# Optimization experiments

Measured on AMD Instinct MI355X. Metric: run time of the kernel, lower is better.

## Reference

```python
import jax, jax.numpy as jnp
import numpy as np

NUM_SLOTS = 3
NUM_ORIENTS = 8
PATCH_SIZE = 81  # 9x9 board
BUY_SIZE = NUM_SLOTS * NUM_ORIENTS * PATCH_SIZE  # 1944
ACTIONS = 1 + PATCH_SIZE + BUY_SIZE  # 2026
NEG = -1.0e9
EPS = 1e-5

B = 4096
C_IN = 256
HID = 256


def setup_inputs() -> dict:
    key = jax.random.key(0)
    ks = jax.random.split(key, 12)
    s = 0.05
    return {
        "x": jax.random.normal(ks[0], (B, C_IN, 9, 9), jnp.float32),
        "action_mask": jax.random.randint(ks[1], (B, ACTIONS), 0, 2, dtype=jnp.int32),
        # p_conv: 1x1 conv, no bias (use_batch_norm=True) -> weight (HID, C_IN)
        "conv_w": jax.random.normal(ks[2], (HID, C_IN), jnp.float32) * s,
        # BatchNorm2d (inference form with running stats)
        "bn_gamma": jnp.ones((HID,), jnp.float32),
        "bn_beta": jnp.zeros((HID,), jnp.float32),
        "bn_mean": jax.random.normal(ks[3], (HID,), jnp.float32) * 0.1,
        "bn_var": jax.random.uniform(ks[4], (HID,), jnp.float32, 0.5, 1.5),
        "type_w": jax.random.normal(ks[5], (3, HID), jnp.float32) * s,
        "type_b": jnp.zeros((3,), jnp.float32),
        "patch_w": jax.random.normal(ks[6], (1, HID), jnp.float32) * s,
        "patch_b": jnp.zeros((1,), jnp.float32),
        "slot_w": jax.random.normal(ks[7], (NUM_SLOTS, HID), jnp.float32) * s,
        "slot_b": jnp.zeros((NUM_SLOTS,), jnp.float32),
        "orient_w": jax.random.normal(ks[8], (NUM_SLOTS * NUM_ORIENTS, HID), jnp.float32) * s,
        "orient_b": jnp.zeros((NUM_SLOTS * NUM_ORIENTS,), jnp.float32),
        "pos_w": jax.random.normal(ks[9], (NUM_SLOTS * NUM_ORIENTS, HID), jnp.float32) * s,
        "pos_b": jnp.zeros((NUM_SLOTS * NUM_ORIENTS,), jnp.float32),
    }


def _masked_logsoftmax(logits, mask_bool):
    lg = jnp.where(mask_bool, logits, NEG)
    return jnp.maximum(jax.nn.log_softmax(lg, axis=-1), -100.0)


def reference(x, action_mask, conv_w, bn_gamma, bn_beta, bn_mean, bn_var,
              type_w, type_b, patch_w, patch_b, slot_w, slot_b,
              orient_w, orient_b, pos_w, pos_b):
    b = x.shape[0]
    # 1x1 conv + BN (eval) + ReLU
    p = jnp.einsum('bchw,oc->bohw', x, conv_w)
    scale = bn_gamma * jax.lax.rsqrt(bn_var + EPS)
    p = jax.nn.relu(p * scale[None, :, None, None] + (bn_beta - bn_mean * scale)[None, :, None, None])
    p_mean = p.mean(axis=(2, 3))  # (B, HID)

    # masks from action_mask layout [pass | 81 patch | 1944 buy]
    am = action_mask > 0
    patch_mask = am[:, 1:1 + PATCH_SIZE]
    buy4d = am[:, 82:82 + BUY_SIZE].reshape(b, NUM_SLOTS, NUM_ORIENTS, PATCH_SIZE)
    type_mask = jnp.stack([am[:, 0], patch_mask.any(-1), buy4d.reshape(b, -1).any(-1)], axis=-1)
    orient_mask = buy4d.any(-1)
    slot_mask = orient_mask.any(-1)

    type_lp = _masked_logsoftmax(p_mean @ type_w.T + type_b, type_mask)          # (B,3)
    patch_logits = jnp.einsum('bchw,oc->bohw', p, patch_w).reshape(b, PATCH_SIZE) \
        + patch_b[0]
    patch_lp = _masked_logsoftmax(patch_logits, patch_mask)                       # (B,81)
    slot_lp = _masked_logsoftmax(p_mean @ slot_w.T + slot_b, slot_mask)           # (B,3)
    orient_lp = _masked_logsoftmax(
        (p_mean @ orient_w.T + orient_b).reshape(b, NUM_SLOTS, NUM_ORIENTS), orient_mask)
    pos_logits = (jnp.einsum('bchw,oc->bohw', p, pos_w) + pos_b[None, :, None, None]) \
        .reshape(b, NUM_SLOTS, NUM_ORIENTS, PATCH_SIZE)
    pos_lp = _masked_logsoftmax(pos_logits, buy4d)                                # (B,3,8,81)

    pass_lp = type_lp[:, 0:1]
    patch_joint = type_lp[:, 1:2] + patch_lp
    buy_joint = (type_lp[:, 2:3, None, None] + slot_lp[:, :, None, None]
                 + orient_lp[:, :, :, None] + pos_lp).reshape(b, BUY_SIZE)
    return jnp.concatenate([pass_lp, patch_joint, buy_joint], axis=1)  # (B, 2026)
```

## Files before the change

### kernel.cpp

```cpp
#include <hip/hip_runtime.h>

#define ACT 2026
#define NEGV -1.0e9f

typedef short short8 __attribute__((ext_vector_type(8)));
typedef float f32x4 __attribute__((ext_vector_type(4)));

__device__ __forceinline__ unsigned f2bf(float f) {
  unsigned u = __float_as_uint(f);
  return (u + 0x7FFFu + ((u >> 16) & 1u)) >> 16;
}

__device__ __forceinline__ unsigned cvtpk(float lo, float hi) {
  unsigned r;
  asm("v_cvt_pk_bf16_f32 %0, %1, %2" : "=v"(r) : "v"(lo), "v"(hi));
  return r;
}

#define GL16(gp, lp) __builtin_amdgcn_global_load_lds(                         \
    (const __attribute__((address_space(1))) void*)(gp),                       \
    (__attribute__((address_space(3))) void*)(lp), 16, 0, 0)

__global__ void prep_w_kernel(const float* __restrict__ conv_w,
                              const float* __restrict__ pos_w,
                              const float* __restrict__ patch_w,
                              unsigned short* __restrict__ wimg,
                              unsigned short* __restrict__ w2img) {
  int g = blockIdx.x * 256 + threadIdx.x;
  if (g < 8192) {
    int r = g & 15, gq = (g >> 4) & 3, mtg = (g >> 6) & 15, ks = g >> 10;
    const float* src = conv_w + (mtg * 16 + r) * 256 + ks * 32 + gq * 8;
    unsigned v0 = f2bf(src[0]) | (f2bf(src[1]) << 16);
    unsigned v1 = f2bf(src[2]) | (f2bf(src[3]) << 16);
    unsigned v2 = f2bf(src[4]) | (f2bf(src[5]) << 16);
    unsigned v3 = f2bf(src[6]) | (f2bf(src[7]) << 16);
    uint4 q; q.x = v0; q.y = v1; q.z = v2; q.w = v3;
    *(uint4*)(wimg + g * 8) = q;
  } else if (g < 9216) {
    int g2 = g - 8192;
    int r = g2 & 15, gq = (g2 >> 4) & 3, mt = (g2 >> 6) & 1, ks2 = g2 >> 7;
    int m2 = mt * 16 + r;
    int o0 = ks2 * 32 + gq * 8;
    unsigned short v[8];
#pragma unroll
    for (int e = 0; e < 8; ++e) {
      float f = 0.f;
      if (m2 < 24) f = pos_w[m2 * 256 + o0 + e];
      else if (m2 == 24) f = patch_w[o0 + e];
      v[e] = (unsigned short)f2bf(f);
    }
    uint4 q;
    q.x = (unsigned)v[0] | ((unsigned)v[1] << 16);
    q.y = (unsigned)v[2] | ((unsigned)v[3] << 16);
    q.z = (unsigned)v[4] | ((unsigned)v[5] << 16);
    q.w = (unsigned)v[6] | ((unsigned)v[7] << 16);
    *(uint4*)(w2img + g2 * 8) = q;
  }
}

__global__ __launch_bounds__(512, 4)
void policy_main(const float* __restrict__ x,
                 const int* __restrict__ am,
                 const unsigned short* __restrict__ wimg,
                 const unsigned short* __restrict__ w2img,
                 const float* __restrict__ bn_gamma, const float* __restrict__ bn_beta,
                 const float* __restrict__ bn_mean, const float* __restrict__ bn_var,
                 const float* __restrict__ type_w, const float* __restrict__ type_b,
                 const float* __restrict__ patch_b,
                 const float* __restrict__ slot_w, const float* __restrict__ slot_b,
                 const float* __restrict__ orient_w, const float* __restrict__ orient_b,
                 const float* __restrict__ pos_b,
                 float* __restrict__ out)
{
  __shared__ __align__(16) char s_big[66048];
  __shared__ __align__(16) float s_scale[256];
  __shared__ __align__(16) float s_bias[256];
  __shared__ __align__(16) float s_pmean[256];
  __shared__ float s_part[240];
  __shared__ float s_hl[30];
  __shared__ int s_omask[24];
  __shared__ int s_misc[6];

  char* f32buf = s_big;
  char* bfimg  = s_big + 41472;
  unsigned short* pT = (unsigned short*)s_big;
  float* s_out2 = (float*)s_big;

  const int tid = threadIdx.x;
  const int w  = tid >> 6;
  const int l  = tid & 63;
  const int b  = blockIdx.x;
  const float* xb = x + (size_t)b * (256 * 81);

  if (tid < 256) {
    float sc = bn_gamma[tid] * rsqrtf(bn_var[tid] + 1e-5f);
    s_scale[tid] = sc;
    s_bias[tid]  = bn_beta[tid] - bn_mean[tid] * sc;
  }

  const int kg = l >> 4;
  const int kr = l & 15;
  const int g4 = kg * 4;
  const int fragoff = (kr * 4 + kg) * 16;

  f32x4 acc[2][6];
#pragma unroll
  for (int i = 0; i < 2; ++i)
#pragma unroll
    for (int j = 0; j < 6; ++j) {
      f32x4 z = {0.f, 0.f, 0.f, 0.f};
      acc[i][j] = z;
    }

  auto STAGE = [&](int ks) {
    const char* g = (const char*)xb + ks * 10368;
    char* lb = f32buf + (ks & 3) * 10368;
    int o1 = w * 81;
    int o2 = o1 + 17;
    GL16(g + (o1 + l) * 16, lb + o1 * 16);
    GL16(g + (o2 + l) * 16, lb + o2 * 16);
  };

  auto TRX = [&](int t, int q) {
    const float* src = (const float*)(f32buf + (t & 3) * 10368);
    char* dst = bfimg + (t & 3) * 6144;
    int nt_ = q >> 6, kr_ = (q >> 2) & 15, kg_ = q & 3;
    const float* s = src + kg_ * 648 + nt_ * 16 + kr_;
    uint4 v;
    v.x = cvtpk(s[0],   s[81]);
    v.y = cvtpk(s[162], s[243]);
    v.z = cvtpk(s[324], s[405]);
    v.w = cvtpk(s[486], s[567]);
    *(uint4*)(dst + q * 16) = v;
  };
  auto TRANSPOSE2 = [&](int tA, int tB) {
    if (tid < 384) TRX(tA, tid);
    else           TRX(tB, tid - 384);
    if (tid < 256) TRX(tB, 128 + tid);
  };

  STAGE(0); STAGE(1); STAGE(2); STAGE(3);
  asm volatile("s_waitcnt vmcnt(4)" ::: "memory");
  __builtin_amdgcn_s_barrier();
  __builtin_amdgcn_sched_barrier(0);
  TRANSPOSE2(0, 1);
  asm volatile("s_waitcnt vmcnt(0)" ::: "memory");
  asm volatile("s_waitcnt lgkmcnt(0)" ::: "memory");
  __builtin_amdgcn_s_barrier();
  __builtin_amdgcn_sched_barrier(0);

  auto SUPER = [&](int s) {
    const int t0 = 2 * s, t1 = t0 + 1;
    short8 af[4];
    {
      const unsigned short* ab0 = wimg + t0 * 8192 + w * 1024 + kg * 128 + kr * 8;
      const unsigned short* ab1 = wimg + t1 * 8192 + w * 1024 + kg * 128 + kr * 8;
      af[0] = *(const short8*)(ab0);
      af[1] = *(const short8*)(ab0 + 512);
      af[2] = *(const short8*)(ab1);
      af[3] = *(const short8*)(ab1 + 512);
    }
    __builtin_amdgcn_sched_barrier(0);
    if (s < 2) {
      STAGE(t0 + 4);
      STAGE(t1 + 4);
    }
    if (s < 3) TRANSPOSE2(t0 + 2, t1 + 2);
    const char* bi0 = bfimg + (t0 & 3) * 6144;
    const char* bi1 = bfimg + (t1 & 3) * 6144;
    __builtin_amdgcn_s_setprio(1);
#pragma unroll
    for (int nt = 0; nt < 6; ++nt) {
      short8 bf = *(const short8*)(bi0 + nt * 1024 + fragoff);
      acc[0][nt] = __builtin_amdgcn_mfma_f32_16x16x32_bf16(af[0], bf, acc[0][nt], 0, 0, 0);
      acc[1][nt] = __builtin_amdgcn_mfma_f32_16x16x32_bf16(af[1], bf, acc[1][nt], 0, 0, 0);
    }
#pragma unroll
    for (int nt = 0; nt < 6; ++nt) {
      short8 bf = *(const short8*)(bi1 + nt * 1024 + fragoff);
      acc[0][nt] = __builtin_amdgcn_mfma_f32_16x16x32_bf16(af[2], bf, acc[0][nt], 0, 0, 0);
      acc[1][nt] = __builtin_amdgcn_mfma_f32_16x16x32_bf16(af[3], bf, acc[1][nt], 0, 0, 0);
    }
    __builtin_amdgcn_s_setprio(0);
    if (s < 3) {
      asm volatile("s_waitcnt vmcnt(0)" ::: "memory");
      asm volatile("s_waitcnt lgkmcnt(0)" ::: "memory");
      __builtin_amdgcn_s_barrier();
      __builtin_amdgcn_sched_barrier(0);
    } else {
      __syncthreads();
    }
  };

  SUPER(0); SUPER(1); SUPER(2); SUPER(3);

#pragma unroll
  for (int mi = 0; mi < 2; ++mi) {
    int ob = w * 32 + mi * 16 + g4;
    float sc0 = s_scale[ob], sc1 = s_scale[ob + 1], sc2 = s_scale[ob + 2], sc3 = s_scale[ob + 3];
    float bi0 = s_bias[ob],  bi1 = s_bias[ob + 1],  bi2 = s_bias[ob + 2],  bi3 = s_bias[ob + 3];
    float vs0 = 0.f, vs1 = 0.f, vs2 = 0.f, vs3 = 0.f;
    int ks2 = ob >> 5;
    int j2  = (ob >> 3) & 3;
    int e0  = ob & 7;
    char* pbase = (char*)pT + ks2 * 6144 + j2 * 256 + kr * 16 + e0 * 2;
#pragma unroll
    for (int nt = 0; nt < 6; ++nt) {
      float v0 = fmaxf(acc[mi][nt][0] * sc0 + bi0, 0.f);
      float v1 = fmaxf(acc[mi][nt][1] * sc1 + bi1, 0.f);
      float v2 = fmaxf(acc[mi][nt][2] * sc2 + bi2, 0.f);
      float v3 = fmaxf(acc[mi][nt][3] * sc3 + bi3, 0.f);
      if (nt < 5 || kr == 0) { vs0 += v0; vs1 += v1; vs2 += v2; vs3 += v3; }
      uint2 pvv;
      pvv.x = cvtpk(v0, v1);
      pvv.y = cvtpk(v2, v3);
      *(uint2*)(pbase + nt * 1024) = pvv;
    }
    float vv[4] = {vs0, vs1, vs2, vs3};
#pragma unroll
    for (int i = 0; i < 4; ++i) {
      float s = vv[i];
      s += __shfl_xor(s, 1);
      s += __shfl_xor(s, 2);
      s += __shfl_xor(s, 4);
      s += __shfl_xor(s, 8);
      vv[i] = s;
    }
    if (kr == 0) {
      s_pmean[ob]     = vv[0] * (1.f / 81.f);
      s_pmean[ob + 1] = vv[1] * (1.f / 81.f);
      s_pmean[ob + 2] = vv[2] * (1.f / 81.f);
      s_pmean[ob + 3] = vv[3] * (1.f / 81.f);
    }
  }
  __syncthreads();

  const int* amr = am + (size_t)b * ACT;
  const int mt  = w & 1;
  const int ntb = (w >> 1) * 3;
  f32x4 acc2[3];
#pragma unroll
  for (int t = 0; t < 3; ++t) { f32x4 z = {0.f, 0.f, 0.f, 0.f}; acc2[t] = z; }

  if (w < 4) {
#pragma unroll
    for (int ks2 = 0; ks2 < 8; ++ks2) {
      const unsigned short* ap = w2img + ((ks2 * 2 + mt) * 4 + kg) * 128 + kr * 8;
      short8 a2 = *(const short8*)ap;
#pragma unroll
      for (int t = 0; t < 3; ++t) {
        const short8* bp = (const short8*)((const char*)pT + ks2 * 6144 + (ntb + t) * 1024 + kg * 256 + kr * 16);
        acc2[t] = __builtin_amdgcn_mfma_f32_16x16x32_bf16(a2, *bp, acc2[t], 0, 0, 0);
      }
    }
  } else {
    for (int t = w - 4; t < 25; t += 4) {
      int off = (t < 24) ? (82 + t * 81) : 1;
      int v1 = amr[off + l];
      int v2 = (l < 17) ? amr[off + 64 + l] : 0;
      unsigned long long bal = __ballot((v1 | v2) != 0);
      if (l == 0) {
        int any = (bal != 0ULL) ? 1 : 0;
        if (t < 24) s_omask[t] = any; else s_misc[0] = any;
      }
    }
    int hh = tid - 256;
    if (hh < 240) {
      int h = hh >> 3, seg = hh & 7;
      const float* wp = (h < 3) ? (type_w + h * 256)
                      : (h < 6) ? (slot_w + (h - 3) * 256)
                                : (orient_w + (h - 6) * 256);
      float p = 0.f;
      int base = seg * 32;
#pragma unroll 8
      for (int e = 0; e < 32; ++e) p += s_pmean[base + e] * wp[base + e];
      s_part[hh] = p;
    }
  }
  __syncthreads();

  if (w < 4) {
#pragma unroll
    for (int t = 0; t < 3; ++t) {
      int hw = (ntb + t) * 16 + kr;
      int m2 = mt * 16 + g4;
#pragma unroll
      for (int i = 0; i < 4; ++i)
        s_out2[(m2 + i) * 104 + hw] = acc2[t][i];
    }
  }
  if (tid < 30) {
    float a = 0.f;
#pragma unroll
    for (int e = 0; e < 8; ++e) a += s_part[tid * 8 + e];
    a += (tid < 3) ? type_b[tid] : (tid < 6) ? slot_b[tid - 3] : orient_b[tid - 6];
    s_hl[tid] = a;
  }
  if (tid == 32) {
    int sa0 = 0, sa1 = 0, sa2 = 0;
#pragma unroll
    for (int rr = 0; rr < 8; ++rr) { sa0 |= s_omask[rr]; sa1 |= s_omask[8 + rr]; sa2 |= s_omask[16 + rr]; }
    s_misc[1] = sa0; s_misc[2] = sa1; s_misc[3] = sa2;
    s_misc[4] = sa0 | sa1 | sa2;
  }
  __syncthreads();

  float tlp0, tlp1, tlp2;
  {
    int mk0 = amr[0] > 0, mk1 = s_misc[0], mk2 = s_misc[4];
    float g0 = mk0 ? s_hl[0] : NEGV;
    float g1 = mk1 ? s_hl[1] : NEGV;
    float g2 = mk2 ? s_hl[2] : NEGV;
    float m = fmaxf(fmaxf(g0, g1), g2);
    float ls = m + __logf(__expf(g0 - m) + __expf(g1 - m) + __expf(g2 - m));
    tlp0 = fmaxf(g0 - ls, -100.f);
    tlp1 = fmaxf(g1 - ls, -100.f);
    tlp2 = fmaxf(g2 - ls, -100.f);
  }
  float slp[3];
  {
    float g[3]; float m = -3.0e38f;
#pragma unroll
    for (int s = 0; s < 3; ++s) { g[s] = s_misc[1 + s] ? s_hl[3 + s] : NEGV; m = fmaxf(m, g[s]); }
    float sum = 0.f;
#pragma unroll
    for (int s = 0; s < 3; ++s) sum += __expf(g[s] - m);
    float ls = m + __logf(sum);
#pragma unroll
    for (int s = 0; s < 3; ++s) slp[s] = fmaxf(g[s] - ls, -100.f);
  }

  float* ob_out = out + (size_t)b * ACT;
  for (int t = w; t < 25; t += 8) {
    int off = (t < 24) ? (82 + t * 81) : 1;
    float badd = (t < 24) ? pos_b[t] : patch_b[0];
    int a1 = amr[off + l];
    int a2v = (l < 17) ? amr[off + 64 + l] : 0;
    float lg1 = (a1 > 0) ? (s_out2[t * 104 + l] + badd) : NEGV;
    float lg2 = (l < 17 && a2v > 0) ? (s_out2[t * 104 + 64 + l] + badd) : NEGV;
    float mx = fmaxf(lg1, (l < 17) ? lg2 : -3.0e38f);
#pragma unroll
    for (int mm = 1; mm < 64; mm <<= 1) mx = fmaxf(mx, __shfl_xor(mx, mm));
    float sm = __expf(lg1 - mx) + ((l < 17) ? __expf(lg2 - mx) : 0.f);
#pragma unroll
    for (int mm = 1; mm < 64; mm <<= 1) sm += __shfl_xor(sm, mm);
    float lse = mx + __logf(sm);
    float lp1 = fmaxf(lg1 - lse, -100.f);
    float lp2 = fmaxf(lg2 - lse, -100.f);
    float addj; int obase;
    if (t < 24) {
      int sl = t >> 3;
      float g[8]; float m = -3.0e38f;
#pragma unroll
      for (int rr = 0; rr < 8; ++rr) {
        g[rr] = s_omask[sl * 8 + rr] ? s_hl[6 + sl * 8 + rr] : NEGV;
        m = fmaxf(m, g[rr]);
      }
      float sum = 0.f;
#pragma unroll
      for (int rr = 0; rr < 8; ++rr) sum += __expf(g[rr] - m);
      float ls = m + __logf(sum);
      float olp_t = fmaxf(g[t & 7] - ls, -100.f);
      addj = tlp2 + slp[sl] + olp_t;
      obase = 82 + t * 81;
    } else {
      addj = tlp1;
      obase = 1;
    }
    ob_out[obase + l] = addj + lp1;
    if (l < 17) ob_out[obase + 64 + l] = addj + lp2;
    if (t == 24 && l == 0) ob_out[0] = tlp0;
  }
}

extern "C" void kernel_launch(void* const* d_in, const int* in_sizes, int n_in,
                              void* d_out, int out_size, void* d_ws, size_t ws_size,
                              hipStream_t stream) {
  (void)in_sizes; (void)n_in; (void)out_size; (void)ws_size;
  const float* x        = (const float*)d_in[0];
  const int*   amask    = (const int*)d_in[1];
  const float* conv_w   = (const float*)d_in[2];
  const float* bn_gamma = (const float*)d_in[3];
  const float* bn_beta  = (const float*)d_in[4];
  const float* bn_mean  = (const float*)d_in[5];
  const float* bn_var   = (const float*)d_in[6];
  const float* type_w   = (const float*)d_in[7];
  const float* type_b   = (const float*)d_in[8];
  const float* patch_w  = (const float*)d_in[9];
  const float* patch_b  = (const float*)d_in[10];
  const float* slot_w   = (const float*)d_in[11];
  const float* slot_b   = (const float*)d_in[12];
  const float* orient_w = (const float*)d_in[13];
  const float* orient_b = (const float*)d_in[14];
  const float* pos_w    = (const float*)d_in[15];
  const float* pos_b    = (const float*)d_in[16];
  float* outp = (float*)d_out;

  unsigned short* wimg  = (unsigned short*)d_ws;
  unsigned short* w2img = wimg + 65536;

  prep_w_kernel<<<36, 256, 0, stream>>>(conv_w, pos_w, patch_w, wimg, w2img);
  policy_main<<<4096, 512, 0, stream>>>(x, amask, wimg, w2img,
                                        bn_gamma, bn_beta, bn_mean, bn_var,
                                        type_w, type_b, patch_b,
                                        slot_w, slot_b, orient_w, orient_b,
                                        pos_b, outp);
}
```

Measured before the change: 193.9 us.

## Double block size to 16 waves, halving per-wave channel tile in conv GEMM

Launches 1024-thread blocks so each of the 16 waves computes 16 output channels instead of 32 in the 1x1-conv MFMA stage. Staging and transpose work are redistributed over the extra threads. Later phases are guarded so only the original wave ranges do the head GEMM and mask reductions. The intent is more resident waves per CU and fewer accumulator registers per wave, to hide load and transpose latency. The cost is that the extra waves sit idle in the tail phases. The tighter launch bound may also force register spills.

New measurement: 186.3 us. 1.04x faster.

```diff
diff --git a/kernel.cpp b/kernel.cpp
--- a/kernel.cpp
+++ b/kernel.cpp
@@ -58,7 +58,7 @@
   }
 }
 
-__global__ __launch_bounds__(512, 4)
+__global__ __launch_bounds__(1024, 8)
 void policy_main(const float* __restrict__ x,
                  const int* __restrict__ am,
                  const unsigned short* __restrict__ wimg,
@@ -103,22 +103,17 @@
   const int g4 = kg * 4;
   const int fragoff = (kr * 4 + kg) * 16;
 
-  f32x4 acc[2][6];
-#pragma unroll
-  for (int i = 0; i < 2; ++i)
-#pragma unroll
-    for (int j = 0; j < 6; ++j) {
-      f32x4 z = {0.f, 0.f, 0.f, 0.f};
-      acc[i][j] = z;
-    }
+  f32x4 acc[6];
+#pragma unroll
+  for (int j = 0; j < 6; ++j) {
+    f32x4 z = {0.f, 0.f, 0.f, 0.f};
+    acc[j] = z;
+  }
 
   auto STAGE = [&](int ks) {
     const char* g = (const char*)xb + ks * 10368;
     char* lb = f32buf + (ks & 3) * 10368;
-    int o1 = w * 81;
-    int o2 = o1 + 17;
-    GL16(g + (o1 + l) * 16, lb + o1 * 16);
-    GL16(g + (o2 + l) * 16, lb + o2 * 16);
+    if (tid < 648) GL16(g + tid * 16, lb + tid * 16);
   };
 
   auto TRX = [&](int t, int q) {
@@ -134,13 +129,12 @@
     *(uint4*)(dst + q * 16) = v;
   };
   auto TRANSPOSE2 = [&](int tA, int tB) {
-    if (tid < 384) TRX(tA, tid);
-    else           TRX(tB, tid - 384);
-    if (tid < 256) TRX(tB, 128 + tid);
+    if (tid < 384)      TRX(tA, tid);
+    else if (tid < 768) TRX(tB, tid - 384);
   };
 
   STAGE(0); STAGE(1); STAGE(2); STAGE(3);
-  asm volatile("s_waitcnt vmcnt(4)" ::: "memory");
+  asm volatile("s_waitcnt vmcnt(2)" ::: "memory");
   __builtin_amdgcn_s_barrier();
   __builtin_amdgcn_sched_barrier(0);
   TRANSPOSE2(0, 1);
@@ -151,14 +145,11 @@
 
   auto SUPER = [&](int s) {
     const int t0 = 2 * s, t1 = t0 + 1;
-    short8 af[4];
+    short8 af0, af1;
     {
-      const unsigned short* ab0 = wimg + t0 * 8192 + w * 1024 + kg * 128 + kr * 8;
-      const unsigned short* ab1 = wimg + t1 * 8192 + w * 1024 + kg * 128 + kr * 8;
-      af[0] = *(const short8*)(ab0);
-      af[1] = *(const short8*)(ab0 + 512);
-      af[2] = *(const short8*)(ab1);
-      af[3] = *(const short8*)(ab1 + 512);
+      const unsigned short* ab = wimg + w * 512 + kg * 128 + kr * 8;
+      af0 = *(const short8*)(ab + t0 * 8192);
+      af1 = *(const short8*)(ab + t1 * 8192);
     }
     __builtin_amdgcn_sched_barrier(0);
     if (s < 2) {
@@ -172,14 +163,12 @@
 #pragma unroll
     for (int nt = 0; nt < 6; ++nt) {
       short8 bf = *(const short8*)(bi0 + nt * 1024 + fragoff);
-      acc[0][nt] = __builtin_amdgcn_mfma_f32_16x16x32_bf16(af[0], bf, acc[0][nt], 0, 0, 0);
-      acc[1][nt] = __builtin_amdgcn_mfma_f32_16x16x32_bf16(af[1], bf, acc[1][nt], 0, 0, 0);
+      acc[nt] = __builtin_amdgcn_mfma_f32_16x16x32_bf16(af0, bf, acc[nt], 0, 0, 0);
     }
 #pragma unroll
     for (int nt = 0; nt < 6; ++nt) {
       short8 bf = *(const short8*)(bi1 + nt * 1024 + fragoff);
-      acc[0][nt] = __builtin_amdgcn_mfma_f32_16x16x32_bf16(af[2], bf, acc[0][nt], 0, 0, 0);
-      acc[1][nt] = __builtin_amdgcn_mfma_f32_16x16x32_bf16(af[3], bf, acc[1][nt], 0, 0, 0);
+      acc[nt] = __builtin_amdgcn_mfma_f32_16x16x32_bf16(af1, bf, acc[nt], 0, 0, 0);
     }
     __builtin_amdgcn_s_setprio(0);
     if (s < 3) {
@@ -194,9 +183,8 @@
 
   SUPER(0); SUPER(1); SUPER(2); SUPER(3);
 
-#pragma unroll
-  for (int mi = 0; mi < 2; ++mi) {
-    int ob = w * 32 + mi * 16 + g4;
+  {
+    int ob = w * 16 + g4;
     float sc0 = s_scale[ob], sc1 = s_scale[ob + 1], sc2 = s_scale[ob + 2], sc3 = s_scale[ob + 3];
     float bi0 = s_bias[ob],  bi1 = s_bias[ob + 1],  bi2 = s_bias[ob + 2],  bi3 = s_bias[ob + 3];
     float vs0 = 0.f, vs1 = 0.f, vs2 = 0.f, vs3 = 0.f;
@@ -206,10 +194,10 @@
     char* pbase = (char*)pT + ks2 * 6144 + j2 * 256 + kr * 16 + e0 * 2;
 #pragma unroll
     for (int nt = 0; nt < 6; ++nt) {
-      float v0 = fmaxf(acc[mi][nt][0] * sc0 + bi0, 0.f);
-      float v1 = fmaxf(acc[mi][nt][1] * sc1 + bi1, 0.f);
-      float v2 = fmaxf(acc[mi][nt][2] * sc2 + bi2, 0.f);
-      float v3 = fmaxf(acc[mi][nt][3] * sc3 + bi3, 0.f);
+      float v0 = fmaxf(acc[nt][0] * sc0 + bi0, 0.f);
+      float v1 = fmaxf(acc[nt][1] * sc1 + bi1, 0.f);
+      float v2 = fmaxf(acc[nt][2] * sc2 + bi2, 0.f);
+      float v3 = fmaxf(acc[nt][3] * sc3 + bi3, 0.f);
       if (nt < 5 || kr == 0) { vs0 += v0; vs1 += v1; vs2 += v2; vs3 += v3; }
       uint2 pvv;
       pvv.x = cvtpk(v0, v1);
@@ -253,7 +241,7 @@
         acc2[t] = __builtin_amdgcn_mfma_f32_16x16x32_bf16(a2, *bp, acc2[t], 0, 0, 0);
       }
     }
-  } else {
+  } else if (w < 8) {
     for (int t = w - 4; t < 25; t += 4) {
       int off = (t < 24) ? (82 + t * 81) : 1;
       int v1 = amr[off + l];
@@ -331,7 +319,7 @@
   }
 
   float* ob_out = out + (size_t)b * ACT;
-  for (int t = w; t < 25; t += 8) {
+  for (int t = w; t < 25; t += 16) {
     int off = (t < 24) ? (82 + t * 81) : 1;
     float badd = (t < 24) ? pos_b[t] : patch_b[0];
     int a1 = amr[off + l];
@@ -400,9 +388,9 @@
   unsigned short* w2img = wimg + 65536;
 
   prep_w_kernel<<<36, 256, 0, stream>>>(conv_w, pos_w, patch_w, wimg, w2img);
-  policy_main<<<4096, 512, 0, stream>>>(x, amask, wimg, w2img,
-                                        bn_gamma, bn_beta, bn_mean, bn_var,
-                                        type_w, type_b, patch_b,
-                                        slot_w, slot_b, orient_w, orient_b,
-                                        pos_b, outp);
-}
+  policy_main<<<4096, 1024, 0, stream>>>(x, amask, wimg, w2img,
+                                         bn_gamma, bn_beta, bn_mean, bn_var,
+                                         type_w, type_b, patch_b,
+                                         slot_w, slot_b, orient_w, orient_b,
+                                         pos_b, outp);
+}
```
